# Optimization experiments

Hardware: AMD Instinct MI355X
Metric: run time of the kernel (lower is better)

The kernel has to match this reference:

```python
import jax, jax.numpy as jnp
import numpy as np
import itertools

BATCH = 8192
NUM_FIELDS = 30
VOCAB = 100000
DIM = 64
ATT_DIM = DIM // 2


def setup_inputs() -> dict:
    key = jax.random.key(0)
    ks = jax.random.split(key, 12)
    x = jax.random.randint(ks[0], (BATCH, NUM_FIELDS), 0, VOCAB)
    emb = jax.random.normal(ks[1], (VOCAB, DIM), dtype=jnp.float32) * 0.05
    W = jax.random.normal(ks[2], (DIM, ATT_DIM), dtype=jnp.float32) * (1.0 / np.sqrt(DIM))
    b = jnp.zeros((ATT_DIM,), dtype=jnp.float32)
    h = jax.random.normal(ks[3], (ATT_DIM,), dtype=jnp.float32) * 0.05
    d1_w = jax.random.normal(ks[4], (DIM // 2, DIM), dtype=jnp.float32) * (1.0 / np.sqrt(DIM))
    d1_b = jnp.zeros((DIM // 2,), dtype=jnp.float32)
    d2_w = jax.random.normal(ks[5], (DIM // 4, DIM // 2), dtype=jnp.float32) * (1.0 / np.sqrt(DIM // 2))
    d2_b = jnp.zeros((DIM // 4,), dtype=jnp.float32)
    ffn_w = jax.random.normal(ks[6], (1, DIM // 4), dtype=jnp.float32) * (1.0 / np.sqrt(DIM // 4))
    ffn_b = jnp.zeros((1,), dtype=jnp.float32)
    return {"x": x, "emb": emb, "W": W, "b": b, "h": h,
            "d1_w": d1_w, "d1_b": d1_b, "d2_w": d2_w, "d2_b": d2_b,
            "ffn_w": ffn_w, "ffn_b": ffn_b}


# static pairwise combination indices over the field axis
_ROW, _COL = map(np.asarray, zip(*itertools.combinations(range(NUM_FIELDS), 2)))


def reference(x, emb, W, b, h, d1_w, d1_b, d2_w, d2_b, ffn_w, ffn_b):
    e = emb[x]                                   # [B, F, D] embedding gather
    half_bip = e[:, _ROW] * e[:, _COL]           # [B, P, D] pairwise products, P=C(F,2)
    att_h = jax.nn.relu(jnp.einsum('bpd,da->bpa', half_bip, W) + b)  # [B, P, A]
    att = jax.nn.softmax(att_h @ h, axis=-1)     # [B, P]
    pooled = jnp.einsum('bpd,bp->bd', half_bip, att)  # attention-weighted sum -> [B, D]
    out = jax.nn.relu(pooled @ d1_w.T + d1_b)    # [B, D/2]
    out = jax.nn.relu(out @ d2_w.T + d2_b)       # [B, D/4]
    logits = jax.nn.sigmoid(out @ ffn_w.T + ffn_b)  # [B, 1]
    return logits
```

## Files before the change

kernel.cpp:

```cpp
#include <hip/hip_runtime.h>
#include <hip/hip_fp16.h>
#include <math.h>

#define NF   30
#define NP   435
#define NPAD 448
#define NT   14
#define DIM  64
#define ATT  32
#define EHS  68
#define WAS  40
#define BPB  4

typedef __attribute__((ext_vector_type(4)))  _Float16 half4v;
typedef __attribute__((ext_vector_type(8)))  _Float16 half8v;
typedef __attribute__((ext_vector_type(16))) float    f32x16;

struct IJTab { unsigned short v[NPAD]; };
static constexpr IJTab make_ij() {
    IJTab t{};
    int p = 0;
    for (int i = 0; i < NF; ++i)
        for (int j = i + 1; j < NF; ++j)
            t.v[p++] = (unsigned short)(i | (j << 8));
    for (; p < NPAD; ++p) t.v[p] = (unsigned short)(31 | (31 << 8));
    return t;
}
__constant__ IJTab IJ = make_ij();

struct __align__(16) WaveCtx {
    _Float16 Eh[32][EHS];
    _Float16 UA[32][WAS];
    float    pooled[DIM];
    float    h1[32];
    float    h2[16];
};

__launch_bounds__(256, 5)
__global__ void afm_wave_kernel(const int*   __restrict__ x,
                                const float* __restrict__ emb,
                                const float* __restrict__ W,
                                const float* __restrict__ bb,
                                const float* __restrict__ hh,
                                const float* __restrict__ d1w,
                                const float* __restrict__ d1b,
                                const float* __restrict__ d2w,
                                const float* __restrict__ d2b,
                                const float* __restrict__ fw,
                                const float* __restrict__ fb,
                                float* __restrict__ out,
                                int Btot)
{
    __shared__ WaveCtx ctx[BPB];
    __shared__ __align__(16) _Float16 Wt[32][WAS];

    const int t    = threadIdx.x;
    const int lane = t & 63;
    const int w    = t >> 6;
    const int col  = lane & 31;
    const int half = lane >> 5;
    const int b    = blockIdx.x * BPB + w;

    WaveCtx& C = ctx[w];

    {
        const int a = t >> 3, kb = (t & 7) * 8;
        half8v w8;
        #pragma unroll
        for (int e = 0; e < 8; ++e) w8[e] = (_Float16)W[(kb + e) * ATT + a];
        *(half8v*)&Wt[a][kb] = w8;
    }
    if (b < Btot) {
        #pragma unroll
        for (int u = lane; u < 256; u += 64) {
            const int row = u >> 3, cb = (u & 7) * 8;
            half4v lo, hi;
            if (row < NF) {
                const int xr = x[b * NF + row];
                const float4 f0 = *(const float4*)&emb[(long)xr * DIM + cb];
                const float4 f1 = *(const float4*)&emb[(long)xr * DIM + cb + 4];
                lo[0] = (_Float16)f0.x; lo[1] = (_Float16)f0.y;
                lo[2] = (_Float16)f0.z; lo[3] = (_Float16)f0.w;
                hi[0] = (_Float16)f1.x; hi[1] = (_Float16)f1.y;
                hi[2] = (_Float16)f1.z; hi[3] = (_Float16)f1.w;
            } else {
                lo = (half4v)(_Float16)0; hi = (half4v)(_Float16)0;
            }
            *(half4v*)&C.Eh[row][cb]     = lo;
            *(half4v*)&C.Eh[row][cb + 4] = hi;
        }
        const float4 z4 = make_float4(0.f, 0.f, 0.f, 0.f);
        #pragma unroll
        for (int idx = lane; idx < 160; idx += 64)
            ((float4*)C.UA)[idx] = z4;
    }
    __syncthreads();

    if (b >= Btot) return;

    half8v wfrag[4];
    #pragma unroll
    for (int ks = 0; ks < 4; ++ks)
        wfrag[ks] = *(const half8v*)&Wt[col][ks * 16 + half * 8];

    float4 b4[4], h4[4];
    #pragma unroll
    for (int q = 0; q < 4; ++q) {
        b4[q] = *(const float4*)&bb[8 * q + 4 * half];
        h4[q] = *(const float4*)&hh[8 * q + 4 * half];
    }

    float wsum = 0.f;
    #pragma unroll 2
    for (int tile = 0; tile < NT; ++tile) {
        const int p  = tile * 32 + col;
        const int pj = IJ.v[p];
        const int fi = pj & 255, fj = pj >> 8;
        f32x16 acc = {};
        #pragma unroll
        for (int ks = 0; ks < 4; ++ks) {
            const int d0 = ks * 16 + half * 8;
            const half4v a0 = *(const half4v*)&C.Eh[fi][d0];
            const half4v a1 = *(const half4v*)&C.Eh[fi][d0 + 4];
            const half4v c0 = *(const half4v*)&C.Eh[fj][d0];
            const half4v c1 = *(const half4v*)&C.Eh[fj][d0 + 4];
            const half4v p0 = a0 * c0;
            const half4v p1 = a1 * c1;
            const half8v bp = __builtin_shufflevector(p0, p1, 0, 1, 2, 3, 4, 5, 6, 7);
            acc = __builtin_amdgcn_mfma_f32_32x32x16_f16(wfrag[ks], bp, acc, 0, 0, 0);
        }
        float sv = 0.f;
        #pragma unroll
        for (int q = 0; q < 4; ++q) {
            sv += fmaxf(acc[4 * q + 0] + b4[q].x, 0.f) * h4[q].x;
            sv += fmaxf(acc[4 * q + 1] + b4[q].y, 0.f) * h4[q].y;
            sv += fmaxf(acc[4 * q + 2] + b4[q].z, 0.f) * h4[q].z;
            sv += fmaxf(acc[4 * q + 3] + b4[q].w, 0.f) * h4[q].w;
        }
        sv += __shfl_xor(sv, 32);
        if (half == 0 && p < NP) {
            const float ex = __expf(sv);
            C.UA[fi][fj] = (_Float16)ex;
            wsum += ex;
        }
    }
    #pragma unroll
    for (int o = 1; o <= 16; o <<= 1) wsum += __shfl_xor(wsum, o);
    const float inv_sum = 1.f / wsum;

    half8v uaf[2];
    uaf[0] = *(const half8v*)&C.UA[col][half * 8];
    uaf[1] = *(const half8v*)&C.UA[col][16 + half * 8];
    #pragma unroll
    for (int dh = 0; dh < 2; ++dh) {
        const int d = col + 32 * dh;
        f32x16 tacc = {};
        #pragma unroll
        for (int ks = 0; ks < 2; ++ks) {
            const int j0 = ks * 16 + half * 8;
            half8v eb;
            #pragma unroll
            for (int e = 0; e < 8; ++e) eb[e] = C.Eh[j0 + e][d];
            tacc = __builtin_amdgcn_mfma_f32_32x32x16_f16(uaf[ks], eb, tacc, 0, 0, 0);
        }
        float sv = 0.f;
        #pragma unroll
        for (int q = 0; q < 4; ++q) {
            const int i0 = 8 * q + 4 * half;
            #pragma unroll
            for (int s = 0; s < 4; ++s)
                sv += (float)C.Eh[i0 + s][d] * tacc[4 * q + s];
        }
        sv += __shfl_xor(sv, 32);
        if (half == 0) C.pooled[d] = sv * inv_sum;
    }

    {
        const int o = lane >> 1, part = lane & 1;
        const float* wr = &d1w[o * DIM + part * 32];
        const float* pp = &C.pooled[part * 32];
        float a1 = 0.f;
        #pragma unroll
        for (int k = 0; k < 32; ++k) a1 = fmaf(pp[k], wr[k], a1);
        a1 += __shfl_xor(a1, 1);
        if (part == 0) C.h1[o] = fmaxf(a1 + d1b[o], 0.f);
    }
    {
        const int o = lane >> 2, part = lane & 3;
        float a2 = 0.f;
        #pragma unroll
        for (int k = 0; k < 8; ++k)
            a2 = fmaf(C.h1[part * 8 + k], d2w[o * 32 + part * 8 + k], a2);
        a2 += __shfl_xor(a2, 1);
        a2 += __shfl_xor(a2, 2);
        if (part == 0) C.h2[o] = fmaxf(a2 + d2b[o], 0.f);
    }
    if (lane < 16) {
        float v = C.h2[lane] * fw[lane];
        #pragma unroll
        for (int o2 = 1; o2 < 16; o2 <<= 1) v += __shfl_xor(v, o2);
        if (lane == 0) out[b] = 1.f / (1.f + __expf(-(v + fb[0])));
    }
}

extern "C" void kernel_launch(void* const* d_in, const int* in_sizes, int n_in,
                              void* d_out, int out_size, void* d_ws, size_t ws_size,
                              hipStream_t stream) {
    (void)n_in; (void)d_ws; (void)ws_size; (void)out_size;
    const int*   x   = (const int*)  d_in[0];
    const float* emb = (const float*)d_in[1];
    const float* W   = (const float*)d_in[2];
    const float* bbp = (const float*)d_in[3];
    const float* hhp = (const float*)d_in[4];
    const float* d1w = (const float*)d_in[5];
    const float* d1b = (const float*)d_in[6];
    const float* d2w = (const float*)d_in[7];
    const float* d2b = (const float*)d_in[8];
    const float* fw  = (const float*)d_in[9];
    const float* fb  = (const float*)d_in[10];
    float* out = (float*)d_out;

    const int B = in_sizes[0] / NF;
    const int grid = (B + BPB - 1) / BPB;
    afm_wave_kernel<<<grid, 256, 0, stream>>>(x, emb, W, bbp, hhp,
                                              d1w, d1b, d2w, d2b, fw, fb, out, B);
}
```

Before: 43.67 us.

## Swizzle LDS layouts, drop block-level sync and shared W staging

Replaces the padded LDS arrays for embeddings and attention scores with XOR-swizzled layouts so 16-byte vector loads avoid bank conflicts without padding. It removes the shared transposed-W buffer and the __syncthreads by having each wave load its W fragment straight from global memory, so every wave works independently. The smaller LDS footprint lets the occupancy hint rise from 5 to 6 blocks. In exchange there are more uncoalesced global reads of W per wave and extra index arithmetic.

```diff
diff --git a/kernel.cpp b/kernel.cpp
--- a/kernel.cpp
+++ b/kernel.cpp
@@ -8,11 +8,8 @@
 #define NT   14
 #define DIM  64
 #define ATT  32
-#define EHS  68
-#define WAS  40
 #define BPB  4
 
-typedef __attribute__((ext_vector_type(4)))  _Float16 half4v;
 typedef __attribute__((ext_vector_type(8)))  _Float16 half8v;
 typedef __attribute__((ext_vector_type(16))) float    f32x16;
 
@@ -28,15 +25,22 @@
 }
 __constant__ IJTab IJ = make_ij();
 
+__device__ __forceinline__ int eh_off(int row, int d) {
+    return (row << 6) + ((((d >> 3) ^ (row & 7)) << 3) | (d & 7));
+}
+__device__ __forceinline__ int ua_off(int i, int j) {
+    return (i << 5) + ((((j >> 3) ^ (i & 7)) << 3) | (j & 7));
+}
+
 struct __align__(16) WaveCtx {
-    _Float16 Eh[32][EHS];
-    _Float16 UA[32][WAS];
+    _Float16 Eh[32 * 64];
+    _Float16 UA[32 * 32];
     float    pooled[DIM];
     float    h1[32];
     float    h2[16];
 };
 
-__launch_bounds__(256, 5)
+__launch_bounds__(256, 6)
 __global__ void afm_wave_kernel(const int*   __restrict__ x,
                                 const float* __restrict__ emb,
                                 const float* __restrict__ W,
@@ -52,7 +56,6 @@
                                 int Btot)
 {
     __shared__ WaveCtx ctx[BPB];
-    __shared__ __align__(16) _Float16 Wt[32][WAS];
 
     const int t    = threadIdx.x;
     const int lane = t & 63;
@@ -61,47 +64,38 @@
     const int half = lane >> 5;
     const int b    = blockIdx.x * BPB + w;
 
+    if (b >= Btot) return;
     WaveCtx& C = ctx[w];
 
+    #pragma unroll
+    for (int it = 0; it < 4; ++it) {
+        const int s = it * 64 + lane;
+        const int row = s >> 3, blk = s & 7;
+        half8v v8 = {};
+        if (row < NF) {
+            const int xr = x[b * NF + row];
+            const float4 f0 = *(const float4*)&emb[(long)xr * DIM + blk * 8];
+            const float4 f1 = *(const float4*)&emb[(long)xr * DIM + blk * 8 + 4];
+            v8[0] = (_Float16)f0.x; v8[1] = (_Float16)f0.y;
+            v8[2] = (_Float16)f0.z; v8[3] = (_Float16)f0.w;
+            v8[4] = (_Float16)f1.x; v8[5] = (_Float16)f1.y;
+            v8[6] = (_Float16)f1.z; v8[7] = (_Float16)f1.w;
+        }
+        *(half8v*)&C.Eh[(row << 6) + ((blk ^ (row & 7)) << 3)] = v8;
+    }
     {
-        const int a = t >> 3, kb = (t & 7) * 8;
-        half8v w8;
-        #pragma unroll
-        for (int e = 0; e < 8; ++e) w8[e] = (_Float16)W[(kb + e) * ATT + a];
-        *(half8v*)&Wt[a][kb] = w8;
-    }
-    if (b < Btot) {
-        #pragma unroll
-        for (int u = lane; u < 256; u += 64) {
-            const int row = u >> 3, cb = (u & 7) * 8;
-            half4v lo, hi;
-            if (row < NF) {
-                const int xr = x[b * NF + row];
-                const float4 f0 = *(const float4*)&emb[(long)xr * DIM + cb];
-                const float4 f1 = *(const float4*)&emb[(long)xr * DIM + cb + 4];
-                lo[0] = (_Float16)f0.x; lo[1] = (_Float16)f0.y;
-                lo[2] = (_Float16)f0.z; lo[3] = (_Float16)f0.w;
-                hi[0] = (_Float16)f1.x; hi[1] = (_Float16)f1.y;
-                hi[2] = (_Float16)f1.z; hi[3] = (_Float16)f1.w;
-            } else {
-                lo = (half4v)(_Float16)0; hi = (half4v)(_Float16)0;
-            }
-            *(half4v*)&C.Eh[row][cb]     = lo;
-            *(half4v*)&C.Eh[row][cb + 4] = hi;
-        }
-        const float4 z4 = make_float4(0.f, 0.f, 0.f, 0.f);
-        #pragma unroll
-        for (int idx = lane; idx < 160; idx += 64)
-            ((float4*)C.UA)[idx] = z4;
-    }
-    __syncthreads();
-
-    if (b >= Btot) return;
+        const float4 z = make_float4(0.f, 0.f, 0.f, 0.f);
+        ((float4*)C.UA)[lane]      = z;
+        ((float4*)C.UA)[lane + 64] = z;
+    }
 
     half8v wfrag[4];
     #pragma unroll
-    for (int ks = 0; ks < 4; ++ks)
-        wfrag[ks] = *(const half8v*)&Wt[col][ks * 16 + half * 8];
+    for (int ks = 0; ks < 4; ++ks) {
+        #pragma unroll
+        for (int e = 0; e < 8; ++e)
+            wfrag[ks][e] = (_Float16)W[(ks * 16 + half * 8 + e) * ATT + col];
+    }
 
     float4 b4[4], h4[4];
     #pragma unroll
@@ -116,17 +110,16 @@
         const int p  = tile * 32 + col;
         const int pj = IJ.v[p];
         const int fi = pj & 255, fj = pj >> 8;
+        const _Float16* Ei = &C.Eh[fi << 6];
+        const _Float16* Ej = &C.Eh[fj << 6];
+        const int si = fi & 7, sj = fj & 7;
         f32x16 acc = {};
         #pragma unroll
         for (int ks = 0; ks < 4; ++ks) {
-            const int d0 = ks * 16 + half * 8;
-            const half4v a0 = *(const half4v*)&C.Eh[fi][d0];
-            const half4v a1 = *(const half4v*)&C.Eh[fi][d0 + 4];
-            const half4v c0 = *(const half4v*)&C.Eh[fj][d0];
-            const half4v c1 = *(const half4v*)&C.Eh[fj][d0 + 4];
-            const half4v p0 = a0 * c0;
-            const half4v p1 = a1 * c1;
-            const half8v bp = __builtin_shufflevector(p0, p1, 0, 1, 2, 3, 4, 5, 6, 7);
+            const int blk = 2 * ks + half;
+            const half8v va = *(const half8v*)&Ei[(blk ^ si) << 3];
+            const half8v vc = *(const half8v*)&Ej[(blk ^ sj) << 3];
+            const half8v bp = va * vc;
             acc = __builtin_amdgcn_mfma_f32_32x32x16_f16(wfrag[ks], bp, acc, 0, 0, 0);
         }
         float sv = 0.f;
@@ -140,7 +133,7 @@
         sv += __shfl_xor(sv, 32);
         if (half == 0 && p < NP) {
             const float ex = __expf(sv);
-            C.UA[fi][fj] = (_Float16)ex;
+            C.UA[ua_off(fi, fj)] = (_Float16)ex;
             wsum += ex;
         }
     }
@@ -149,8 +142,9 @@
     const float inv_sum = 1.f / wsum;
 
     half8v uaf[2];
-    uaf[0] = *(const half8v*)&C.UA[col][half * 8];
-    uaf[1] = *(const half8v*)&C.UA[col][16 + half * 8];
+    #pragma unroll
+    for (int ks = 0; ks < 2; ++ks)
+        uaf[ks] = *(const half8v*)&C.UA[(col << 5) + (((2 * ks + half) ^ (col & 7)) << 3)];
     #pragma unroll
     for (int dh = 0; dh < 2; ++dh) {
         const int d = col + 32 * dh;
@@ -160,7 +154,7 @@
             const int j0 = ks * 16 + half * 8;
             half8v eb;
             #pragma unroll
-            for (int e = 0; e < 8; ++e) eb[e] = C.Eh[j0 + e][d];
+            for (int e = 0; e < 8; ++e) eb[e] = C.Eh[eh_off(j0 + e, d)];
             tacc = __builtin_amdgcn_mfma_f32_32x32x16_f16(uaf[ks], eb, tacc, 0, 0, 0);
         }
         float sv = 0.f;
@@ -169,7 +163,7 @@
             const int i0 = 8 * q + 4 * half;
             #pragma unroll
             for (int s = 0; s < 4; ++s)
-                sv += (float)C.Eh[i0 + s][d] * tacc[4 * q + s];
+                sv += (float)C.Eh[eh_off(i0 + s, d)] * tacc[4 * q + s];
         }
         sv += __shfl_xor(sv, 32);
         if (half == 0) C.pooled[d] = sv * inv_sum;
```

After: 75.71 us. +73.4%, slower.
